# Kernel optimization log

Measured on AMD Instinct MI355X. Metric: run time of the kernel, lower is better.

## Reference

```python
import jax, jax.numpy as jnp
import numpy as np

# Fixed-shape Conformer chunked attention (Gemma3n audio style)
S = 8192          # seq_len
H = 16            # num_heads
D = 128           # head_dim
HD = H * D        # hidden size = 2048
C = 12            # chunk_size
MP = 12           # max_past_horizon
MF = 0            # max_future_horizon
CTX = C + MP + MF # context_size = 24
POS = MP + MF + 1 # pos_length = 13
N = (S + C - 1) // C            # num_blocks
PAD = N * C - S                 # pad_amount
Q_SCALE = D ** -0.5 * 1.4426950408889634  # head_dim**-0.5 / softplus(0)
SOFTCAP = 50.0


def setup_inputs() -> dict:
    key = jax.random.key(0)
    ks = jax.random.split(key, 8)
    w = lambda k, shape: jax.random.normal(k, shape, jnp.float32) * 0.02
    return {
        "hidden_states": jax.random.normal(ks[0], (1, S, HD), jnp.float32),
        "position_embeddings": jax.random.normal(ks[1], (POS, HD), jnp.float32),
        "Wq": w(ks[2], (HD, HD)),
        "Wk": w(ks[3], (HD, HD)),
        "Wv": w(ks[4], (HD, HD)),
        "W_rel": w(ks[5], (HD, HD)),
        "W_post": w(ks[6], (HD, HD)),
        "per_dim_scale": jax.random.normal(ks[7], (D,), jnp.float32) * 0.1,
    }


def reference(hidden_states, position_embeddings, Wq, Wk, Wv, W_rel, W_post, per_dim_scale):
    x = hidden_states[0]  # [S, HD]
    q = (x @ Wq).reshape(S, H, D) * (Q_SCALE * jax.nn.softplus(per_dim_scale))
    k = (x @ Wk).reshape(S, H, D)  # k_scale = 1.0
    v = (x @ Wv).reshape(S, H, D)

    # query blocks [N, C, H, D]
    qb = jnp.pad(q, ((0, PAD), (0, 0), (0, 0))).reshape(N, C, H, D)
    # key/value padded then gathered into sliding context blocks [N, CTX, H, D]
    kp = jnp.pad(k, ((MP, MF + C - 1), (0, 0), (0, 0)))
    vp = jnp.pad(v, ((MP, MF + C - 1), (0, 0), (0, 0)))
    idx = jnp.arange(N)[:, None] * C + jnp.arange(CTX)[None, :]  # [N, CTX]
    kb = kp[idx]
    vb = vp[idx]

    rel_k = (position_embeddings @ W_rel).reshape(POS, H, D)

    # content scores [H, N, C, CTX]
    ac = jnp.einsum('nchd,nkhd->hnck', qb, kb)
    # relative-position scores via shift trick
    bd = jnp.einsum('nchd,phd->hncp', qb, rel_k)          # [H, N, C, POS]
    bd = jnp.pad(bd, ((0, 0), (0, 0), (0, 0), (0, CTX + 1 - POS)))
    bd = bd.reshape(H, N, C * (CTX + 1))[:, :, :C * CTX].reshape(H, N, C, CTX)

    attn = jnp.tanh((ac + bd) / SOFTCAP) * SOFTCAP        # softcap
    attn = jax.nn.softmax(attn, axis=-1)

    out = jnp.einsum('hnck,nkhd->nchd', attn, vb).reshape(N * C, HD)[:S]
    return (out @ W_post)[None]  # [1, S, HD]
```

## Files before the change

### kernel.cpp

```cpp
#include <hip/hip_runtime.h>
#include <hip/hip_bf16.h>

#define S_LEN 8192
#define NH    16
#define HD    128
#define HID   2048
#define NQKV  6144
#define CHUNK 12
#define MP    12
#define CTX   24
#define POS   13
#define NBLK  683

typedef short bf16x8 __attribute__((ext_vector_type(8)));
typedef float f32x4  __attribute__((ext_vector_type(4)));
typedef unsigned short u16;
typedef u16 u16x8 __attribute__((ext_vector_type(8)));
typedef u16 u16x4 __attribute__((ext_vector_type(4)));

#define MFMA16 __builtin_amdgcn_mfma_f32_16x16x32_bf16

__device__ __forceinline__ void glds16(const u16* g, u16* l) {
  __builtin_amdgcn_global_load_lds(
      (__attribute__((address_space(1))) void*)(void*)g,
      (__attribute__((address_space(3))) void*)l, 16, 0, 0);
}

__device__ __forceinline__ u16 f2b(float f) {
  __hip_bfloat16 h = __float2bfloat16(f);
  return *(u16*)&h;
}

__global__ __launch_bounds__(256) void f32_to_bf16(const float* __restrict__ in,
                                                   u16* __restrict__ out, int n) {
  int i = (blockIdx.x * 256 + threadIdx.x) * 4;
  if (i < n) {
    float4 v = *(const float4*)(in + i);
    u16x4 o = {f2b(v.x), f2b(v.y), f2b(v.z), f2b(v.w)};
    *(u16x4*)(out + i) = o;
  }
}

__global__ __launch_bounds__(256) void transpose4(const float* __restrict__ W0,
                                                  const float* __restrict__ W1,
                                                  const float* __restrict__ W2,
                                                  const float* __restrict__ W3,
                                                  u16* __restrict__ out) {
  __shared__ u16 t[64][72];
  const int z = blockIdx.z;
  const float* in = (z == 0) ? W0 : (z == 1) ? W1 : (z == 2) ? W2 : W3;
  u16* dst = out + (size_t)z * HID * HID;
  const int bx = blockIdx.x * 64, by = blockIdx.y * 64;
  const int x = threadIdx.x & 63;
  const int y4 = threadIdx.x >> 6;
  for (int r = y4; r < 64; r += 4)
    t[r][x] = f2b(in[(size_t)(by + r) * HID + bx + x]);
  __syncthreads();
  for (int r = y4; r < 64; r += 4)
    dst[(size_t)(bx + r) * HID + by + x] = t[x][r];
}

__global__ void qscale_kernel(const float* __restrict__ pds, float* __restrict__ qs) {
  int d = threadIdx.x;
  float x = pds[d];
  float sp = log1pf(expf(x));
  qs[d] = 0.08838834764831845f * 1.4426950408889634f * sp;
}

__global__ __launch_bounds__(256) void relk_atomic(const float* __restrict__ pos,
                                                   const float* __restrict__ Wrel,
                                                   float* __restrict__ RELF) {
  const int col = blockIdx.x * 256 + threadIdx.x;
  const int c0 = blockIdx.y * 256;
  float acc[POS] = {};
  for (int c = c0; c < c0 + 256; ++c) {
    float wv = Wrel[(size_t)c * HID + col];
#pragma unroll
    for (int p = 0; p < POS; ++p) acc[p] += pos[p * HID + c] * wv;
  }
#pragma unroll
  for (int p = 0; p < POS; ++p) atomicAdd(&RELF[p * HID + col], acc[p]);
}

__global__ __launch_bounds__(256) void relk_cvt(const float* __restrict__ RELF,
                                                u16* __restrict__ REL) {
  int i = blockIdx.x * 256 + threadIdx.x;
  if (i < POS * HID) REL[i] = f2b(RELF[i]);
}

#define BMT 256
#define BNT 256
#define BKT 32
#define NT  (HID / BKT)

__global__ __launch_bounds__(512, 2) void gemm_bt(const u16* __restrict__ A,
                                                  const u16* __restrict__ Bt,
                                                  u16* __restrict__ Co,
                                                  float* __restrict__ Cf,
                                                  const float* __restrict__ colscale,
                                                  int NN, int csLimit) {
  __shared__ u16 lds[4][2][BMT * BKT];
  const int tid = threadIdx.x;
  const int lane = tid & 63, w = tid >> 6;
  const int quad = lane >> 4, l = lane & 15;
  const int wm = (w >> 2) * 128, wn = (w & 3) * 64;

  const int orig = blockIdx.y * gridDim.x + blockIdx.x;
  const int xcd = orig & 7, k = orig >> 3;
  const int bm = (xcd * 4 + (k & 3)) * BMT;
  const int bn = (k >> 2) * BNT;

  const int rdoff = (l >> 1) * 64 + (((((l & 1) << 2) | quad)) ^ ((l >> 1) & 7)) * 8;

  const int sl = (lane & 7) ^ (lane >> 3);
  const int srow = ((lane >> 3) << 1) + (sl >> 2);
  const int sk = (sl & 3) * 8;
  const u16* Ag0 = A + (size_t)(bm + w * 32 + srow) * HID + sk;
  const u16* Ag1 = Ag0 + (size_t)16 * HID;
  const u16* Bg0 = Bt + (size_t)(bn + w * 32 + srow) * HID + sk;
  const u16* Bg1 = Bg0 + (size_t)16 * HID;

  f32x4 acc[8][4] = {};

#pragma unroll
  for (int pt = 0; pt < 3; ++pt) {
    u16* sA = &lds[pt][0][w * 1024];
    u16* sB = &lds[pt][1][w * 1024];
    glds16(Ag0 + pt * BKT, sA);
    glds16(Ag1 + pt * BKT, sA + 512);
    glds16(Bg0 + pt * BKT, sB);
    glds16(Bg1 + pt * BKT, sB + 512);
  }
  asm volatile("s_waitcnt vmcnt(8)");
  __builtin_amdgcn_s_barrier();

#pragma unroll 1
  for (int t = 0; t < NT; ++t) {
    const u16* bufA = &lds[t & 3][0][0];
    const u16* bufB = &lds[t & 3][1][0];
    u16* stA = &lds[(t + 3) & 3][0][w * 1024];
    u16* stB = &lds[(t + 3) & 3][1][w * 1024];
    const int kt = (t + 3) * BKT;
    const bool doStage = (t < NT - 3);

    bf16x8 af[4], bfr[4];
#pragma unroll
    for (int i = 0; i < 4; ++i)
      af[i] = *(const bf16x8*)(bufA + (wm + i * 16) * 32 + rdoff);
#pragma unroll
    for (int j = 0; j < 4; ++j)
      bfr[j] = *(const bf16x8*)(bufB + (wn + j * 16) * 32 + rdoff);
    if (doStage) {
      glds16(Ag0 + kt, stA);
      glds16(Ag1 + kt, stA + 512);
    }
    __builtin_amdgcn_s_barrier();
    __builtin_amdgcn_s_setprio(1);
#pragma unroll
    for (int i = 0; i < 4; ++i)
#pragma unroll
      for (int j = 0; j < 4; ++j)
        acc[i][j] = MFMA16(af[i], bfr[j], acc[i][j], 0, 0, 0);
    __builtin_amdgcn_s_setprio(0);
    __builtin_amdgcn_s_barrier();

#pragma unroll
    for (int i = 0; i < 4; ++i)
      af[i] = *(const bf16x8*)(bufA + (wm + 64 + i * 16) * 32 + rdoff);
    if (doStage) {
      glds16(Bg0 + kt, stB);
      glds16(Bg1 + kt, stB + 512);
    }
    if (t < NT - 3)       asm volatile("s_waitcnt vmcnt(8)");
    else if (t == NT - 3) asm volatile("s_waitcnt vmcnt(4)");
    else if (t == NT - 2) asm volatile("s_waitcnt vmcnt(0)");
    __builtin_amdgcn_s_barrier();
    __builtin_amdgcn_s_setprio(1);
#pragma unroll
    for (int i = 0; i < 4; ++i)
#pragma unroll
      for (int j = 0; j < 4; ++j)
        acc[4 + i][j] = MFMA16(af[i], bfr[j], acc[4 + i][j], 0, 0, 0);
    __builtin_amdgcn_s_setprio(0);
    __builtin_amdgcn_s_barrier();
  }

#pragma unroll
  for (int i = 0; i < 8; ++i)
#pragma unroll
    for (int j = 0; j < 4; ++j)
#pragma unroll
      for (int r = 0; r < 4; ++r) {
        int row = bm + wm + i * 16 + quad * 4 + r;
        int col = bn + wn + j * 16 + l;
        float v = acc[i][j][r];
        if (colscale && col < csLimit) v *= colscale[col & (HD - 1)];
        if (Cf) Cf[(size_t)row * NN + col] = v;
        else    Co[(size_t)row * NN + col] = f2b(v);
      }
}

__global__ __launch_bounds__(64) void attn_kernel(const u16* __restrict__ qkv,
                                                  const u16* __restrict__ relg,
                                                  u16* __restrict__ og) {
  __shared__ char smem[13824];
  u16* qs = (u16*)smem;
  u16* ks = (u16*)(smem + 4352);
  u16* vt = (u16*)smem;
  u16* ps = (u16*)(smem + 12288);
  const int n = blockIdx.x, h = blockIdx.y;
  const int lane = threadIdx.x;
  const int quad = lane >> 4, l = lane & 15;
  const int base = n * CHUNK;
  const u16x8 zero8 = {0, 0, 0, 0, 0, 0, 0, 0};

  const u16* qg = qkv + h * HD;
  const u16* kg = qkv + 2048 + h * HD;
  const u16* vg = qkv + 4096 + h * HD;

  u16x8 vld[8];
#pragma unroll
  for (int i = 0; i < 8; ++i) {
    int id = lane + 64 * i;
    int ctx = id & 31, dc = id >> 5;
    int s = base + ctx - MP;
    vld[i] = (ctx < CTX && s >= 0 && s < S_LEN)
                 ? *(const u16x8*)(vg + (size_t)s * NQKV + dc * 8)
                 : zero8;
  }

#pragma unroll
  for (int i = 0; i < 4; ++i) {
    int id = lane + 64 * i;
    int c = id >> 4, dc = id & 15;
    int s = base + c;
    u16x8 v = (c < CHUNK && s < S_LEN)
                  ? *(const u16x8*)(qg + (size_t)s * NQKV + dc * 8)
                  : zero8;
    *(u16x8*)(qs + c * 136 + dc * 8) = v;
  }
#pragma unroll
  for (int i = 0; i < 8; ++i) {
    int id = lane + 64 * i;
    int ctx = id >> 4, dc = id & 15;
    int s = base + ctx - MP;
    u16x8 v = (ctx < CTX && s >= 0 && s < S_LEN)
                  ? *(const u16x8*)(kg + (size_t)s * NQKV + dc * 8)
                  : zero8;
    *(u16x8*)(ks + ctx * 136 + dc * 8) = v;
  }
  __syncthreads();

  f32x4 ac0 = {0, 0, 0, 0}, ac1 = {0, 0, 0, 0}, bd = {0, 0, 0, 0};
#pragma unroll
  for (int t = 0; t < 4; ++t) {
    int d0 = t * 32;
    bf16x8 aQ = *(const bf16x8*)(qs + l * 136 + d0 + quad * 8);
    bf16x8 bK0 = *(const bf16x8*)(ks + l * 136 + d0 + quad * 8);
    bf16x8 bK1 = *(const bf16x8*)(ks + (16 + l) * 136 + d0 + quad * 8);
    bf16x8 bR = {0, 0, 0, 0, 0, 0, 0, 0};
    if (l < POS)
      bR = *(const bf16x8*)(relg + (size_t)l * HID + h * HD + d0 + quad * 8);
    ac0 = MFMA16(aQ, bK0, ac0, 0, 0, 0);
    ac1 = MFMA16(aQ, bK1, ac1, 0, 0, 0);
    bd = MFMA16(aQ, bR, bd, 0, 0, 0);
  }

  float p0[4], p1[4];
#pragma unroll
  for (int r = 0; r < 4; ++r) {
    int c = quad * 4 + r;
    int pi0 = l - c;
    int pi1 = 16 + l - c;
    int sp0 = pi0 < 0 ? 0 : (pi0 > 15 ? 15 : pi0);
    int sp1 = pi1 < 0 ? 0 : (pi1 > 15 ? 15 : pi1);
    float b0 = __shfl(bd[r], quad * 16 + sp0, 64);
    float b1 = __shfl(bd[r], quad * 16 + sp1, 64);
    b0 = (pi0 >= 0 && pi0 < POS) ? b0 : 0.0f;
    b1 = (pi1 >= 0 && pi1 < POS) ? b1 : 0.0f;
    float s0 = tanhf((ac0[r] + b0) * (1.0f / 50.0f)) * 50.0f;
    float s1 = tanhf((ac1[r] + b1) * (1.0f / 50.0f)) * 50.0f;
    bool v1 = (l < (CTX - 16));
    if (!v1) s1 = -1e30f;
    float mx = fmaxf(s0, s1);
#pragma unroll
    for (int d = 1; d < 16; d <<= 1) mx = fmaxf(mx, __shfl_xor(mx, d, 64));
    float e0 = __expf(s0 - mx);
    float e1 = v1 ? __expf(s1 - mx) : 0.0f;
    float sm = e0 + e1;
#pragma unroll
    for (int d = 1; d < 16; d <<= 1) sm += __shfl_xor(sm, d, 64);
    float inv = 1.0f / sm;
    p0[r] = e0 * inv;
    p1[r] = e1 * inv;
  }
  __syncthreads();

#pragma unroll
  for (int i = 0; i < 8; ++i) {
    int id = lane + 64 * i;
    int ctx = id & 31, dc = id >> 5;
#pragma unroll
    for (int jj = 0; jj < 8; ++jj) vt[(dc * 8 + jj) * 48 + ctx] = vld[i][jj];
  }
#pragma unroll
  for (int r = 0; r < 4; ++r) {
    int c = quad * 4 + r;
    ps[c * 48 + l] = f2b(p0[r]);
    ps[c * 48 + 16 + l] = f2b(p1[r]);
  }
  __syncthreads();

  bf16x8 aP = *(const bf16x8*)(ps + l * 48 + quad * 8);
#pragma unroll
  for (int nt = 0; nt < 8; ++nt) {
    bf16x8 bV = *(const bf16x8*)(vt + (nt * 16 + l) * 48 + quad * 8);
    f32x4 o = {0, 0, 0, 0};
    o = MFMA16(aP, bV, o, 0, 0, 0);
#pragma unroll
    for (int r = 0; r < 4; ++r) {
      int c = quad * 4 + r;
      int s = base + c;
      if (c < CHUNK && s < S_LEN)
        og[(size_t)s * HID + h * HD + nt * 16 + l] = f2b(o[r]);
    }
  }
}

extern "C" void kernel_launch(void* const* d_in, const int* in_sizes, int n_in,
                              void* d_out, int out_size, void* d_ws, size_t ws_size,
                              hipStream_t stream) {
  const float* x = (const float*)d_in[0];
  const float* pos = (const float*)d_in[1];
  const float* Wq = (const float*)d_in[2];
  const float* Wk = (const float*)d_in[3];
  const float* Wv = (const float*)d_in[4];
  const float* Wrel = (const float*)d_in[5];
  const float* Wpost = (const float*)d_in[6];
  const float* pds = (const float*)d_in[7];

  char* ws = (char*)d_ws;
  u16* WT  = (u16*)(ws);
  u16* xb  = (u16*)(ws + 33554432);
  u16* AO  = xb;
  u16* QKV = (u16*)(ws + 67108864);
  float* RELF = (float*)(ws + 167772160);
  u16* REL = (u16*)(ws + 167878656);
  float* QS = (float*)(ws + 167931904);

  const int NX = S_LEN * HID;
  f32_to_bf16<<<NX / 4 / 256, 256, 0, stream>>>(x, xb, NX);

  transpose4<<<dim3(32, 32, 4), 256, 0, stream>>>(Wq, Wk, Wv, Wpost, WT);
  qscale_kernel<<<1, 128, 0, stream>>>(pds, QS);

  hipMemsetAsync(RELF, 0, POS * HID * sizeof(float), stream);
  relk_atomic<<<dim3(8, 8), 256, 0, stream>>>(pos, Wrel, RELF);
  relk_cvt<<<(POS * HID + 255) / 256, 256, 0, stream>>>(RELF, REL);

  gemm_bt<<<dim3(32, 24), 512, 0, stream>>>(xb, WT, QKV, nullptr, QS, NQKV, 2048);

  attn_kernel<<<dim3(NBLK, NH), 64, 0, stream>>>(QKV, REL, AO);

  gemm_bt<<<dim3(32, 8), 512, 0, stream>>>(AO, WT + (size_t)3 * HID * HID,
                                           nullptr, (float*)d_out, nullptr, HID, 0);
}
```

Measured before the change: 597.8 us.

## Prefetch next-tile LDS fragments during MFMAs and cut GEMM barriers

Restructures the bf16 GEMM main loop so the A/B register fragments for the next K tile are read from LDS while the second half of the current tile's MFMAs runs. It also drops from four workgroup barriers per iteration to one, using explicit lgkmcnt/vmcnt waits and sched_barrier to order things. The goal is to hide LDS read latency and synchronisation stalls behind matrix math. In exchange it holds more live VGPRs and leans on the 4-deep buffer ring to avoid overwrite races with fewer barriers.

```diff
diff --git a/kernel.cpp b/kernel.cpp
--- a/kernel.cpp
+++ b/kernel.cpp
@@ -131,58 +131,75 @@
     glds16(Bg0 + pt * BKT, sB);
     glds16(Bg1 + pt * BKT, sB + 512);
   }
-  asm volatile("s_waitcnt vmcnt(8)");
+  asm volatile("s_waitcnt vmcnt(8)" ::: "memory");
   __builtin_amdgcn_s_barrier();
+
+  bf16x8 afC[4], bfC[4], afN[4], bfN[4];
+#pragma unroll
+  for (int i = 0; i < 4; ++i)
+    afC[i] = *(const bf16x8*)(&lds[0][0][0] + (wm + i * 16) * 32 + rdoff);
+#pragma unroll
+  for (int j = 0; j < 4; ++j)
+    bfC[j] = *(const bf16x8*)(&lds[0][1][0] + (wn + j * 16) * 32 + rdoff);
 
 #pragma unroll 1
   for (int t = 0; t < NT; ++t) {
     const u16* bufA = &lds[t & 3][0][0];
-    const u16* bufB = &lds[t & 3][1][0];
     u16* stA = &lds[(t + 3) & 3][0][w * 1024];
     u16* stB = &lds[(t + 3) & 3][1][w * 1024];
     const int kt = (t + 3) * BKT;
     const bool doStage = (t < NT - 3);
 
-    bf16x8 af[4], bfr[4];
-#pragma unroll
-    for (int i = 0; i < 4; ++i)
-      af[i] = *(const bf16x8*)(bufA + (wm + i * 16) * 32 + rdoff);
-#pragma unroll
-    for (int j = 0; j < 4; ++j)
-      bfr[j] = *(const bf16x8*)(bufB + (wn + j * 16) * 32 + rdoff);
     if (doStage) {
       glds16(Ag0 + kt, stA);
       glds16(Ag1 + kt, stA + 512);
     }
-    __builtin_amdgcn_s_barrier();
+    bf16x8 af1[4];
+#pragma unroll
+    for (int i = 0; i < 4; ++i)
+      af1[i] = *(const bf16x8*)(bufA + (wm + 64 + i * 16) * 32 + rdoff);
+    asm volatile("s_waitcnt lgkmcnt(4)" ::: "memory");
+    __builtin_amdgcn_sched_barrier(0);
     __builtin_amdgcn_s_setprio(1);
 #pragma unroll
     for (int i = 0; i < 4; ++i)
 #pragma unroll
       for (int j = 0; j < 4; ++j)
-        acc[i][j] = MFMA16(af[i], bfr[j], acc[i][j], 0, 0, 0);
+        acc[i][j] = MFMA16(afC[i], bfC[j], acc[i][j], 0, 0, 0);
     __builtin_amdgcn_s_setprio(0);
-    __builtin_amdgcn_s_barrier();
-
-#pragma unroll
-    for (int i = 0; i < 4; ++i)
-      af[i] = *(const bf16x8*)(bufA + (wm + 64 + i * 16) * 32 + rdoff);
+
     if (doStage) {
       glds16(Bg0 + kt, stB);
       glds16(Bg1 + kt, stB + 512);
     }
-    if (t < NT - 3)       asm volatile("s_waitcnt vmcnt(8)");
-    else if (t == NT - 3) asm volatile("s_waitcnt vmcnt(4)");
-    else if (t == NT - 2) asm volatile("s_waitcnt vmcnt(0)");
-    __builtin_amdgcn_s_barrier();
+    asm volatile("s_waitcnt lgkmcnt(0)" ::: "memory");
+    if (t < NT - 3)       asm volatile("s_waitcnt vmcnt(8)" ::: "memory");
+    else if (t == NT - 3) asm volatile("s_waitcnt vmcnt(4)" ::: "memory");
+    else if (t == NT - 2) asm volatile("s_waitcnt vmcnt(0)" ::: "memory");
+    __builtin_amdgcn_sched_barrier(0);
+    if (t < NT - 1) {
+      __builtin_amdgcn_s_barrier();
+      const u16* nA = &lds[(t + 1) & 3][0][0];
+      const u16* nB = &lds[(t + 1) & 3][1][0];
+#pragma unroll
+      for (int i = 0; i < 4; ++i)
+        afN[i] = *(const bf16x8*)(nA + (wm + i * 16) * 32 + rdoff);
+#pragma unroll
+      for (int j = 0; j < 4; ++j)
+        bfN[j] = *(const bf16x8*)(nB + (wn + j * 16) * 32 + rdoff);
+    }
     __builtin_amdgcn_s_setprio(1);
 #pragma unroll
     for (int i = 0; i < 4; ++i)
 #pragma unroll
       for (int j = 0; j < 4; ++j)
-        acc[4 + i][j] = MFMA16(af[i], bfr[j], acc[4 + i][j], 0, 0, 0);
+        acc[4 + i][j] = MFMA16(af1[i], bfC[j], acc[4 + i][j], 0, 0, 0);
     __builtin_amdgcn_s_setprio(0);
-    __builtin_amdgcn_s_barrier();
+#pragma unroll
+    for (int r = 0; r < 4; ++r) {
+      afC[r] = afN[r];
+      bfC[r] = bfN[r];
+    }
   }
 
 #pragma unroll
```

Result: faster. 570.6 us (-4.6%).
